# Kernel optimization log

Hardware: AMD Instinct MI355X
Metric: run time of the kernel (lower is better)

## Reference

```python
import jax, jax.numpy as jnp
import numpy as np

SEQ_LEN, BATCH, NUM_GROUPS, GROUP = 12, 512, 16, 32
H, E, MLP, BOTTLE, PRE = 128, 64, 1024, 1024, 512


def _pool_net(h, pos, num_groups, Wp, bp, W1, b1, W2, b2):
    # PoolHiddenNet: for each scene group, pairwise relative positions -> MLP -> max over neighbors
    B = h.shape[0]
    G = B // num_groups
    hg = h.reshape(num_groups, G, -1)          # (NG, G, H)
    pg = pos.reshape(num_groups, G, 2)         # (NG, G, 2)
    rel = pg[:, None, :, :] - pg[:, :, None, :]  # [g,i,j] = pos_j - pos_i
    emb = rel @ Wp.T + bp                      # (NG, G, G, E)
    hj = jnp.broadcast_to(hg[:, None, :, :], (num_groups, G, G, hg.shape[-1]))
    feats = jnp.concatenate([emb, hj], axis=-1)  # (NG, G, G, E+H)
    x = jax.nn.relu(feats @ W1.T + b1)         # (NG, G, G, 512)
    x = jax.nn.relu(x @ W2.T + b2)             # (NG, G, G, 1024)
    return x.max(axis=2).reshape(B, -1)        # max over neighbors j


def setup_inputs() -> dict:
    key = jax.random.key(0)
    ks = jax.random.split(key, 24)
    s = 0.05
    starts = np.arange(NUM_GROUPS, dtype=np.int64) * GROUP
    seq_start_end = jnp.asarray(np.stack([starts, starts + GROUP], axis=1))
    return {
        "last_pos": jax.random.normal(ks[0], (BATCH, 2), jnp.float32),
        "last_pos_rel": jax.random.normal(ks[1], (BATCH, 2), jnp.float32),
        "hh": jax.random.normal(ks[2], (1, BATCH, H), jnp.float32),
        "ch": jax.random.normal(ks[3], (1, BATCH, H), jnp.float32),
        "pred_traj_rel": jax.random.normal(ks[4], (SEQ_LEN, BATCH, 2), jnp.float32),
        "seq_start_end": seq_start_end,
        # LSTM (torch layout: gates ordered i,f,g,o)
        "W_ih": jax.random.normal(ks[5], (4 * H, E), jnp.float32) * s,
        "W_hh": jax.random.normal(ks[6], (4 * H, H), jnp.float32) * s,
        "b_ih": jax.random.normal(ks[7], (4 * H,), jnp.float32) * s,
        "b_hh": jax.random.normal(ks[8], (4 * H,), jnp.float32) * s,
        # spatial_embedding Linear(2, E)
        "Wse": jax.random.normal(ks[9], (E, 2), jnp.float32) * s,
        "bse": jax.random.normal(ks[10], (E,), jnp.float32) * s,
        # hidden2pos Linear(H, 2)
        "Wpos": jax.random.normal(ks[11], (2, H), jnp.float32) * s,
        "bpos": jax.random.normal(ks[12], (2,), jnp.float32) * s,
        # pool_net spatial_embedding Linear(2, E)
        "Wp": jax.random.normal(ks[13], (E, 2), jnp.float32) * s,
        "bp": jax.random.normal(ks[14], (E,), jnp.float32) * s,
        # pool_net mlp_pre_pool: [E+H, 512, BOTTLE], relu after each linear
        "W1": jax.random.normal(ks[15], (PRE, E + H), jnp.float32) * s,
        "b1": jax.random.normal(ks[16], (PRE,), jnp.float32) * s,
        "W2": jax.random.normal(ks[17], (BOTTLE, PRE), jnp.float32) * s,
        "b2": jax.random.normal(ks[18], (BOTTLE,), jnp.float32) * s,
        # decoder mlp: [H+BOTTLE, MLP, H], relu after each linear
        "Wm1": jax.random.normal(ks[19], (MLP, H + BOTTLE), jnp.float32) * s,
        "bm1": jax.random.normal(ks[20], (MLP,), jnp.float32) * s,
        "Wm2": jax.random.normal(ks[21], (H, MLP), jnp.float32) * s,
        "bm2": jax.random.normal(ks[22], (H,), jnp.float32) * s,
    }


def reference(last_pos, last_pos_rel, hh, ch, pred_traj_rel, seq_start_end,
              W_ih, W_hh, b_ih, b_hh, Wse, bse, Wpos, bpos,
              Wp, bp, W1, b1, W2, b2, Wm1, bm1, Wm2, bm2):
    num_groups = seq_start_end.shape[0]
    h0, c0 = hh[0], ch[0]
    dec_in0 = last_pos_rel @ Wse.T + bse

    def step(carry, gt_rel):
        last_pos_c, h, c, dec_in, loss = carry
        # single-layer LSTM cell (torch gate order i,f,g,o)
        gates = dec_in @ W_ih.T + b_ih + h @ W_hh.T + b_hh
        i, f, g, o = jnp.split(gates, 4, axis=-1)
        c = jax.nn.sigmoid(f) * c + jax.nn.sigmoid(i) * jnp.tanh(g)
        h = jax.nn.sigmoid(o) * jnp.tanh(c)
        rel_pos = h @ Wpos.T + bpos
        curr_pos = rel_pos + last_pos_c
        # pool every timestep + mlp back down to h_dim, replaces hidden state
        pool_h = _pool_net(h, curr_pos, num_groups, Wp, bp, W1, b1, W2, b2)
        dh = jnp.concatenate([h, pool_h], axis=1)
        dh = jax.nn.relu(dh @ Wm1.T + bm1)
        h = jax.nn.relu(dh @ Wm2.T + bm2)
        # training mode: teacher forcing + MSE loss
        loss = loss + jnp.mean((rel_pos - gt_rel) ** 2)
        dec_in = gt_rel @ Wse.T + bse
        return (curr_pos, h, c, dec_in, loss), rel_pos

    init = (last_pos, h0, c0, dec_in0, jnp.float32(0.0))
    (_, _, _, _, loss), pred_traj = jax.lax.scan(step, init, pred_traj_rel)
    return pred_traj, loss
```

## Files before the change

### kernel.cpp

```cpp
#include <hip/hip_runtime.h>
#include <math.h>

#define BATCH 512
#define NG 16
#define GSZ 32
#define H 128
#define E 64
#define PRE 512
#define BOT 1024
#define MLPD 1024
#define SEQ 12
#define AK 1152

typedef __attribute__((ext_vector_type(8))) short bf16x8;
typedef __attribute__((ext_vector_type(4))) float f32x4;

union bf8pack { ushort s[8]; uint4 v; };

__device__ __forceinline__ unsigned short f2bf(float f) {
    unsigned u = __float_as_uint(f);
    u += 0x7FFF + ((u >> 16) & 1);
    return (unsigned short)(u >> 16);
}

__device__ __forceinline__ uint4 pack8(const float* s) {
    float4 a = *(const float4*)s, b = *(const float4*)(s + 4);
    bf8pack o;
    o.s[0] = f2bf(a.x); o.s[1] = f2bf(a.y); o.s[2] = f2bf(a.z); o.s[3] = f2bf(a.w);
    o.s[4] = f2bf(b.x); o.s[5] = f2bf(b.y); o.s[6] = f2bf(b.z); o.s[7] = f2bf(b.w);
    return o.v;
}

#define GLB(p) ((const __attribute__((address_space(1))) unsigned int*)(p))
#define LDS(p) ((__attribute__((address_space(3))) unsigned int*)(p))

#define U0 ((BOT * PRE) / 8)
#define U1 ((MLPD * AK) / 8)
#define U2 ((H * MLPD) / 8)
#define U3 ((PRE * H) / 8)
#define U4 (PRE)
#define U5 ((BATCH * H) / 4)
#define U5b ((BATCH * H) / 8)
#define U6 (BATCH * 2)
#define U7 ((512 * 128) / 8)
#define U8 (512)
#define PREP_TOT (U0 + U1 + U2 + U3 + U4 + U5 + U5b + U6 + U7 + U8 + 1)

__global__ void prep_kernel(
    const float* __restrict__ W2, const float* __restrict__ Wm1,
    const float* __restrict__ Wm2, const float* __restrict__ W1,
    const float* __restrict__ Wp, const float* __restrict__ bp, const float* __restrict__ b1,
    const float* __restrict__ ch, const float* __restrict__ hh, const float* __restrict__ last_pos,
    const float* __restrict__ Wih, const float* __restrict__ Whh,
    const float* __restrict__ bih, const float* __restrict__ bhh,
    const float* __restrict__ Wse, const float* __restrict__ bse,
    unsigned short* __restrict__ W2pk, unsigned short* __restrict__ Wm1pk,
    unsigned short* __restrict__ Wm2pk, unsigned short* __restrict__ W1pk,
    float* __restrict__ Wcx, float* __restrict__ Wcy, float* __restrict__ biash,
    float* __restrict__ cbuf, unsigned short* __restrict__ Ahpk, float* __restrict__ pos,
    unsigned short* __restrict__ Whpk,
    float* __restrict__ Wx0, float* __restrict__ Wx1, float* __restrict__ bx,
    float* __restrict__ loss)
{
    long idx = (long)blockIdx.x * 256 + threadIdx.x;
    if (idx < U0) {
        int u = (int)idx;
        int lane = u & 63, rest = u >> 6;
        int ksg = rest & 15, cg = rest >> 4;
        int col = cg * 16 + (lane & 15);
        int kk = ksg * 32 + (lane >> 4) * 8;
        *(uint4*)&W2pk[(size_t)u * 8] = pack8(&W2[(size_t)col * PRE + kk]);
        return;
    }
    idx -= U0;
    if (idx < U1) {
        int u = (int)idx;
        int lane = u & 63, rest = u >> 6;
        int ksg = rest % 36, cg = rest / 36;
        int col = cg * 16 + (lane & 15);
        int k = ksg * 32 + (lane >> 4) * 8;
        *(uint4*)&Wm1pk[(size_t)u * 8] = pack8(&Wm1[(size_t)col * AK + k]);
        return;
    }
    idx -= U1;
    if (idx < U2) {
        int u = (int)idx;
        int lane = u & 63, rest = u >> 6;
        int ksg = rest & 31, cg = rest >> 5;
        int col = cg * 16 + (lane & 15);
        int k = ksg * 32 + (lane >> 4) * 8;
        *(uint4*)&Wm2pk[(size_t)u * 8] = pack8(&Wm2[(size_t)col * MLPD + k]);
        return;
    }
    idx -= U2;
    if (idx < U3) {
        int u = (int)idx;
        int l16 = u & 15, quad = (u >> 4) & 3, nt = (u >> 6) & 3, ks = (u >> 8) & 3, w = u >> 10;
        int col = w * 64 + nt * 16 + l16;
        int k = ks * 32 + quad * 8;
        *(uint4*)&W1pk[(size_t)u * 8] = pack8(&W1[col * 192 + E + k]);
        return;
    }
    idx -= U3;
    if (idx < U4) {
        int p = (int)idx;
        float sx = 0.f, sy = 0.f, sb = 0.f;
#pragma unroll 8
        for (int e = 0; e < E; ++e) {
            float w = W1[p * 192 + e];
            sx += w * Wp[e * 2 + 0];
            sy += w * Wp[e * 2 + 1];
            sb += w * bp[e];
        }
        Wcx[p] = sx; Wcy[p] = sy; biash[p] = b1[p] + sb;
        return;
    }
    idx -= U4;
    if (idx < U5) { ((float4*)cbuf)[idx] = ((const float4*)ch)[idx]; return; }
    idx -= U5;
    if (idx < U5b) {
        int u = (int)idx;
        int lane = u & 63, rest = u >> 6;
        int ks = rest & 3, rowtile = rest >> 2;
        int row = rowtile * 16 + (lane & 15);
        int k = ks * 32 + (lane >> 4) * 8;
        *(uint4*)&Ahpk[(size_t)u * 8] = pack8(&hh[(size_t)row * H + k]);
        return;
    }
    idx -= U5b;
    if (idx < U6) { pos[idx] = last_pos[idx]; return; }
    idx -= U6;
    if (idx < U7) {
        int u = (int)idx;
        int l16 = u & 15, quad = (u >> 4) & 3, ks = (u >> 6) & 3, w = (u >> 8) & 7, g = u >> 11;
        int col = g * 128 + w * 16 + l16;
        int k = ks * 32 + quad * 8;
        *(uint4*)&Whpk[(size_t)u * 8] = pack8(&Whh[(size_t)col * H + k]);
        return;
    }
    idx -= U7;
    if (idx < U8) {
        int u = (int)idx;
        float sx = 0.f, sy = 0.f, sb = 0.f;
#pragma unroll 8
        for (int e = 0; e < E; ++e) {
            float w = Wih[u * E + e];
            sx += w * Wse[e * 2 + 0];
            sy += w * Wse[e * 2 + 1];
            sb += w * bse[e];
        }
        Wx0[u] = sx; Wx1[u] = sy; bx[u] = sb + bih[u] + bhh[u];
        return;
    }
    idx -= U8;
    if (idx == 0) *loss = 0.0f;
}

#define LROWS 16
__global__ __launch_bounds__(512) void lstm_hpart(
    int t,
    const float* __restrict__ relin, const float* __restrict__ gt,
    const unsigned short* __restrict__ Whpk,
    const float* __restrict__ Wx0, const float* __restrict__ Wx1, const float* __restrict__ bx,
    const float* __restrict__ Wpos, const float* __restrict__ bpos,
    const unsigned short* __restrict__ W1pk, const float* __restrict__ biash,
    const unsigned short* __restrict__ Ahpk, float* __restrict__ cbuf,
    unsigned short* __restrict__ Abf, float* __restrict__ Hpartf,
    float* __restrict__ pos, float* __restrict__ traj, float* __restrict__ loss)
{
    constexpr int LDHB = 136;
    constexpr int LDHF = 129;
    __shared__ __align__(16) unsigned short hnb[LROWS * LDHB];
    __shared__ float hnf[LROWS * LDHF];
    __shared__ float lred[8];
    const int blk = blockIdx.x;
    const int r0 = blk * LROWS;
    const int tid = threadIdx.x;
    const int lane = tid & 63, w = tid >> 6;
    const int quad = lane >> 4, l16 = lane & 15;

    f32x4 acc[4];
#pragma unroll
    for (int g4 = 0; g4 < 4; ++g4) acc[g4] = (f32x4)0.f;
#pragma unroll
    for (int ks = 0; ks < 4; ++ks) {
        bf16x8 af = *(const bf16x8*)&Ahpk[((size_t)(blk * 4 + ks) * 64 + lane) * 8];
#pragma unroll
        for (int gate = 0; gate < 4; ++gate) {
            bf16x8 bf = *(const bf16x8*)&Whpk[((size_t)((gate * 8 + w) * 4 + ks) * 64 + lane) * 8];
            acc[gate] = __builtin_amdgcn_mfma_f32_16x16x32_bf16(af, bf, acc[gate], 0, 0, 0);
        }
    }

    {
        int u = w * 16 + l16;
        float wx0[4], wx1[4], bxv[4];
#pragma unroll
        for (int gate = 0; gate < 4; ++gate) {
            int col = gate * 128 + u;
            wx0[gate] = Wx0[col]; wx1[gate] = Wx1[col]; bxv[gate] = bx[col];
        }
#pragma unroll
        for (int r = 0; r < 4; ++r) {
            int row = quad * 4 + r;
            int b = r0 + row;
            float rx = relin[b * 2 + 0], ry = relin[b * 2 + 1];
            float i_ = acc[0][r] + rx * wx0[0] + ry * wx1[0] + bxv[0];
            float f_ = acc[1][r] + rx * wx0[1] + ry * wx1[1] + bxv[1];
            float g_ = acc[2][r] + rx * wx0[2] + ry * wx1[2] + bxv[2];
            float o_ = acc[3][r] + rx * wx0[3] + ry * wx1[3] + bxv[3];
            float ig = 1.0f / (1.0f + expf(-i_));
            float fg = 1.0f / (1.0f + expf(-f_));
            float gg = tanhf(g_);
            float og = 1.0f / (1.0f + expf(-o_));
            float c = fg * cbuf[(size_t)b * H + u] + ig * gg;
            cbuf[(size_t)b * H + u] = c;
            float h = og * tanhf(c);
            hnb[row * LDHB + u] = f2bf(h);
            hnf[row * LDHF + u] = h;
            Abf[(size_t)b * AK + u] = f2bf(h);
        }
    }
    __syncthreads();

    if (t < SEQ - 1) {
        f32x4 acc2[4];
#pragma unroll
        for (int nt = 0; nt < 4; ++nt) acc2[nt] = (f32x4)0.f;
#pragma unroll
        for (int ks = 0; ks < 4; ++ks) {
            bf16x8 af = *(const bf16x8*)&hnb[l16 * LDHB + ks * 32 + quad * 8];
#pragma unroll
            for (int nt = 0; nt < 4; ++nt) {
                bf16x8 bfr = *(const bf16x8*)&W1pk[((size_t)((w * 4 + ks) * 4 + nt) * 64 + lane) * 8];
                acc2[nt] = __builtin_amdgcn_mfma_f32_16x16x32_bf16(af, bfr, acc2[nt], 0, 0, 0);
            }
        }
#pragma unroll
        for (int nt = 0; nt < 4; ++nt) {
            int col = w * 64 + nt * 16 + l16;
            float bv = biash[col];
#pragma unroll
            for (int r = 0; r < 4; ++r) {
                int row = quad * 4 + r;
                Hpartf[(size_t)(r0 + row) * PRE + col] = acc2[nt][r] + bv;
            }
        }
    }

    {
        int row = tid >> 5, o = (tid >> 4) & 1, seg = tid & 15;
        const float* wr = Wpos + o * H + seg * 8;
        const float* hr = &hnf[row * LDHF + seg * 8];
        float acc3 = 0.f;
#pragma unroll
        for (int k = 0; k < 8; ++k) acc3 += wr[k] * hr[k];
        acc3 += __shfl_xor(acc3, 1);
        acc3 += __shfl_xor(acc3, 2);
        acc3 += __shfl_xor(acc3, 4);
        acc3 += __shfl_xor(acc3, 8);
        acc3 += bpos[o];
        int b = r0 + row;
        float d = acc3 - gt[b * 2 + o];
        if (seg == 0) {
            float lp = pos[b * 2 + o];
            pos[b * 2 + o] = acc3 + lp;
            traj[b * 2 + o] = acc3;
        }
        float part = (seg == 0) ? d * d : 0.f;
        part += __shfl_xor(part, 16);
        part += __shfl_xor(part, 32);
        if (lane == 0) lred[w] = part;
        __syncthreads();
        if (tid == 0) {
            float s = 0.f;
#pragma unroll
            for (int i = 0; i < 8; ++i) s += lred[i];
            atomicAdd(loss, s * (1.0f / 1024.0f));
        }
    }
}

template <int BM, int BN, int KW, int NW, int MODE>
__global__ __launch_bounds__(256) void gemm_splitk_pk(
    const unsigned short* __restrict__ A, int lda,
    const unsigned short* __restrict__ Bpk, int K,
    const float* __restrict__ bias,
    float* __restrict__ Cf, unsigned short* __restrict__ Cb, int ldc)
{
    constexpr int MT = BM / 16;
    constexpr int NT = BN / (16 * NW);
    constexpr int ABUF = KW * BM * 64;
    __shared__ __align__(16) unsigned short As[2 * ABUF];
    __shared__ float red[KW * BM * BN];
    int tid = threadIdx.x;
    int lane = tid & 63, w = tid >> 6;
    int kslice = w / NW, nslice = w % NW;
    int gtid = tid & (NW * 64 - 1);
    int quad = lane >> 4, l16 = lane & 15;
    int m0 = blockIdx.y * BM, n0 = blockIdx.x * BN;
    const int KC = K / KW;
    const int NK = KC / 64;
    const int KSGT = K >> 5;
    const int cgbase = (n0 + nslice * (BN / NW)) >> 4;

    auto STAGE = [&](int ki, int bo) {
        int kb = kslice * KC + ki * 64;
#pragma unroll
        for (int u = 0; u < BM / (8 * NW); ++u) {
            int c = u * NW * 64 + gtid;
            __builtin_amdgcn_global_load_lds(
                GLB(A + (size_t)(m0 + (c >> 3)) * lda + kb + (c & 7) * 8),
                LDS(&As[bo + kslice * BM * 64 + c * 8]), 16, 0, 0);
        }
    };

    f32x4 acc[MT][NT];
#pragma unroll
    for (int mt = 0; mt < MT; ++mt)
#pragma unroll
        for (int nt = 0; nt < NT; ++nt) acc[mt][nt] = (f32x4)0.f;

    STAGE(0, 0);
    for (int ki = 0; ki < NK; ++ki) {
        int bo = (ki & 1) * ABUF;
        int kgbase = (kslice * KC + ki * 64) >> 5;
        __syncthreads();
#pragma unroll
        for (int ks = 0; ks < 2; ++ks) {
            bf16x8 af[MT], bfr[NT];
#pragma unroll
            for (int mt = 0; mt < MT; ++mt)
                af[mt] = *(const bf16x8*)&As[bo + kslice * BM * 64 + (mt * 16 + l16) * 64 + ks * 32 + quad * 8];
#pragma unroll
            for (int nt = 0; nt < NT; ++nt)
                bfr[nt] = *(const bf16x8*)&Bpk[((size_t)((cgbase + nt) * KSGT + kgbase + ks) * 64 + lane) * 8];
#pragma unroll
            for (int mt = 0; mt < MT; ++mt)
#pragma unroll
                for (int nt = 0; nt < NT; ++nt)
                    acc[mt][nt] = __builtin_amdgcn_mfma_f32_16x16x32_bf16(af[mt], bfr[nt], acc[mt][nt], 0, 0, 0);
        }
        if (ki + 1 < NK) STAGE(ki + 1, ((ki + 1) & 1) * ABUF);
    }

#pragma unroll
    for (int mt = 0; mt < MT; ++mt)
#pragma unroll
    for (int nt = 0; nt < NT; ++nt) {
#pragma unroll
        for (int r = 0; r < 4; ++r) {
            int row = mt * 16 + quad * 4 + r;
            int col = nslice * (BN / NW) + nt * 16 + l16;
            red[kslice * BM * BN + row * BN + col] = acc[mt][nt][r];
        }
    }
    __syncthreads();

#pragma unroll
    for (int o = 0; o < BM * BN / 256; ++o) {
        int e = o * 256 + tid;
        int row = e / BN, col = e % BN;
        float s = 0.f;
#pragma unroll
        for (int k = 0; k < KW; ++k) s += red[k * BM * BN + e];
        float v = fmaxf(s + bias[n0 + col], 0.f);
        if (MODE == 1) {
            Cb[(size_t)(m0 + row) * ldc + n0 + col] = f2bf(v);
        } else if (MODE == 2) {
            Cf[(size_t)(m0 + row) * ldc + n0 + col] = v;
        } else {
            int gr = m0 + row, gc = n0 + col;
            int rowtile = gr >> 4, l16p = gr & 15;
            int ksv = gc >> 5, quadp = (gc >> 3) & 3, ep = gc & 7;
            int lanep = quadp * 16 + l16p;
            Cb[((size_t)(rowtile * 4 + ksv) * 64 + lanep) * 8 + ep] = f2bf(v);
        }
    }
}

__global__ __launch_bounds__(512) void pool_fused(
    const float* __restrict__ Hpartf, const float* __restrict__ pos,
    const float* __restrict__ Wcx, const float* __restrict__ Wcy,
    const unsigned short* __restrict__ W2pk,
    const float* __restrict__ b2, unsigned short* __restrict__ Abf)
{
    constexpr int LDA = 72;
    constexpr int ASZ = 128 * LDA;
    __shared__ __align__(16) unsigned short As[2 * ASZ];
    const int tid = threadIdx.x;
    const int lane = tid & 63, w = tid >> 6;
    const int quad = lane >> 4, l16 = lane & 15;
    const int n_tile = blockIdx.x, m_tile = blockIdx.y;
    const int g = m_tile >> 3, iq = m_tile & 7;
    const int n0 = n_tile * 512;

    const int brow = tid >> 2;
    const int k8 = (tid & 3) * 16;
    const int bi = iq * 4 + (brow >> 5), bj = brow & 31;
    const float rx = pos[(g * GSZ + bj) * 2 + 0] - pos[(g * GSZ + bi) * 2 + 0];
    const float ry = pos[(g * GSZ + bj) * 2 + 1] - pos[(g * GSZ + bi) * 2 + 1];
    const float* hrow = &Hpartf[(size_t)(g * GSZ + bj) * PRE];

    auto BUILD = [&](int k0i, unsigned short* dst) {
        const int k0 = k0i * 64;
        const float4* hp = (const float4*)(hrow + k0 + k8);
        const float4* wx = (const float4*)(Wcx + k0 + k8);
        const float4* wy = (const float4*)(Wcy + k0 + k8);
        bf8pack o[2];
#pragma unroll
        for (int q = 0; q < 2; ++q) {
            float4 ha = hp[q * 2], hb = hp[q * 2 + 1];
            float4 xa = wx[q * 2], xb = wx[q * 2 + 1];
            float4 ya = wy[q * 2], yb = wy[q * 2 + 1];
            o[q].s[0] = f2bf(fmaxf(ha.x + rx * xa.x + ry * ya.x, 0.f));
            o[q].s[1] = f2bf(fmaxf(ha.y + rx * xa.y + ry * ya.y, 0.f));
            o[q].s[2] = f2bf(fmaxf(ha.z + rx * xa.z + ry * ya.z, 0.f));
            o[q].s[3] = f2bf(fmaxf(ha.w + rx * xa.w + ry * ya.w, 0.f));
            o[q].s[4] = f2bf(fmaxf(hb.x + rx * xb.x + ry * yb.x, 0.f));
            o[q].s[5] = f2bf(fmaxf(hb.y + rx * xb.y + ry * yb.y, 0.f));
            o[q].s[6] = f2bf(fmaxf(hb.z + rx * xb.z + ry * yb.z, 0.f));
            o[q].s[7] = f2bf(fmaxf(hb.w + rx * xb.w + ry * yb.w, 0.f));
        }
        *(uint4*)&dst[brow * LDA + k8] = o[0].v;
        *(uint4*)&dst[brow * LDA + k8 + 8] = o[1].v;
    };

    f32x4 acc[8][4];
#pragma unroll
    for (int mt = 0; mt < 8; ++mt)
#pragma unroll
        for (int nt = 0; nt < 4; ++nt) acc[mt][nt] = (f32x4)0.f;

    BUILD(0, As);
    for (int k0i = 0; k0i < 8; ++k0i) {
        unsigned short* cur = As + (k0i & 1) * ASZ;
        __syncthreads();
        __builtin_amdgcn_s_setprio(1);
#pragma unroll
        for (int ks = 0; ks < 2; ++ks) {
            bf16x8 bfr[4];
#pragma unroll
            for (int nt = 0; nt < 4; ++nt) {
                int cg = n_tile * 32 + w * 4 + nt;
                int ksg = k0i * 2 + ks;
                bfr[nt] = *(const bf16x8*)&W2pk[((size_t)(cg * 16 + ksg) * 64 + lane) * 8];
            }
#pragma unroll
            for (int mt = 0; mt < 8; ++mt) {
                bf16x8 af = *(const bf16x8*)&cur[(mt * 16 + l16) * LDA + ks * 32 + quad * 8];
#pragma unroll
                for (int nt = 0; nt < 4; ++nt)
                    acc[mt][nt] = __builtin_amdgcn_mfma_f32_16x16x32_bf16(af, bfr[nt], acc[mt][nt], 0, 0, 0);
            }
        }
        __builtin_amdgcn_s_setprio(0);
        if (k0i < 7) BUILD(k0i + 1, As + ((k0i + 1) & 1) * ASZ);
    }

#pragma unroll
    for (int il = 0; il < 4; ++il)
#pragma unroll
    for (int nt = 0; nt < 4; ++nt) {
        float u = -1e30f;
#pragma unroll
        for (int p = 0; p < 2; ++p)
#pragma unroll
            for (int r = 0; r < 4; ++r) u = fmaxf(u, acc[il * 2 + p][nt][r]);
        u = fmaxf(u, __shfl_xor(u, 16));
        u = fmaxf(u, __shfl_xor(u, 32));
        if (lane < 16) {
            int col = n0 + w * 64 + nt * 16 + l16;
            int gu = m_tile * 4 + il;
            Abf[(size_t)gu * AK + H + col] = f2bf(fmaxf(u + b2[col], 0.f));
        }
    }
}

extern "C" void kernel_launch(void* const* d_in, const int* in_sizes, int n_in,
                              void* d_out, int out_size, void* d_ws, size_t ws_size,
                              hipStream_t stream)
{
    const float* last_pos     = (const float*)d_in[0];
    const float* last_pos_rel = (const float*)d_in[1];
    const float* hh           = (const float*)d_in[2];
    const float* ch           = (const float*)d_in[3];
    const float* ptr_rel      = (const float*)d_in[4];
    const float* Wih  = (const float*)d_in[6];
    const float* Whh  = (const float*)d_in[7];
    const float* bih  = (const float*)d_in[8];
    const float* bhh  = (const float*)d_in[9];
    const float* Wse  = (const float*)d_in[10];
    const float* bse  = (const float*)d_in[11];
    const float* Wpos = (const float*)d_in[12];
    const float* bpos = (const float*)d_in[13];
    const float* Wp   = (const float*)d_in[14];
    const float* bp   = (const float*)d_in[15];
    const float* W1   = (const float*)d_in[16];
    const float* b1   = (const float*)d_in[17];
    const float* W2   = (const float*)d_in[18];
    const float* b2   = (const float*)d_in[19];
    const float* Wm1  = (const float*)d_in[20];
    const float* bm1  = (const float*)d_in[21];
    const float* Wm2  = (const float*)d_in[22];
    const float* bm2  = (const float*)d_in[23];

    float* ws     = (float*)d_ws;
    unsigned short* Ahpk = (unsigned short*)ws;
    float* cbuf   = ws + BATCH * H;
    float* pos    = cbuf + BATCH * H;
    float* Hpartf = pos + 1024;
    float* Wcx    = Hpartf + BATCH * PRE;
    float* Wcy    = Wcx + PRE;
    float* biash  = Wcy + PRE;
    float* bx     = biash + PRE;
    float* Wx0    = bx + 512;
    float* Wx1    = Wx0 + 512;
    unsigned short* ub    = (unsigned short*)(Wx1 + 512);
    unsigned short* Abf   = ub;
    unsigned short* dhbf  = Abf + (size_t)BATCH * AK;
    unsigned short* W2pk  = dhbf + (size_t)BATCH * MLPD;
    unsigned short* Wm1pk = W2pk + (size_t)BOT * PRE;
    unsigned short* Wm2pk = Wm1pk + (size_t)MLPD * AK;
    unsigned short* W1pk  = Wm2pk + (size_t)H * MLPD;
    unsigned short* Whpk  = W1pk + (size_t)PRE * H;

    float* out  = (float*)d_out;
    float* loss = out + SEQ * BATCH * 2;

    prep_kernel<<<(PREP_TOT + 255) / 256, 256, 0, stream>>>(
        W2, Wm1, Wm2, W1, Wp, bp, b1, ch, hh, last_pos, Wih, Whh, bih, bhh, Wse, bse,
        W2pk, Wm1pk, Wm2pk, W1pk, Wcx, Wcy, biash, cbuf, Ahpk, pos, Whpk, Wx0, Wx1, bx, loss);

    for (int t = 0; t < SEQ; t++) {
        const float* relin = (t == 0) ? last_pos_rel : (ptr_rel + (t - 1) * BATCH * 2);
        const float* gt = ptr_rel + t * BATCH * 2;
        lstm_hpart<<<BATCH / LROWS, 512, 0, stream>>>(t, relin, gt, Whpk, Wx0, Wx1, bx,
                                                      Wpos, bpos, W1pk, biash, Ahpk, cbuf,
                                                      Abf, Hpartf, pos,
                                                      out + t * BATCH * 2, loss);
        if (t == SEQ - 1) break;
        pool_fused<<<dim3(2, 128), 512, 0, stream>>>(Hpartf, pos, Wcx, Wcy, W2pk, b2, Abf);
        gemm_splitk_pk<64, 32, 2, 2, 1><<<dim3(MLPD / 32, BATCH / 64), 256, 0, stream>>>(
            Abf, AK, Wm1pk, AK, bm1, nullptr, dhbf, MLPD);
        gemm_splitk_pk<16, 32, 4, 1, 3><<<dim3(H / 32, BATCH / 16), 256, 0, stream>>>(
            dhbf, MLPD, Wm2pk, MLPD, bm2, nullptr, Ahpk, H);
    }
}
```

Before: 665.1 us.

## Fuse second MLP GEMM into next-step LSTM kernel to drop a launch

Folds the Wm2 GEMM (dh -> h) into the following timestep's LSTM kernel. Each 16-row block now computes its new hidden state with MFMA over the full K=1024 and stages it in shared memory, so the packed hidden-state round trip through global memory and one kernel launch per step go away. The Wm1 GEMM now writes its output in MFMA-packed layout, which needed the packed-store index to use ldc. The cost is more serial K-loop work per block with no split-K, and each block reloads the Wm2 weights.

```diff
diff --git a/kernel.cpp b/kernel.cpp
--- a/kernel.cpp
+++ b/kernel.cpp
@@ -156,35 +156,26 @@
     if (idx == 0) *loss = 0.0f;
 }
 
-#define LROWS 16
-__global__ __launch_bounds__(512) void lstm_hpart(
-    int t,
-    const float* __restrict__ relin, const float* __restrict__ gt,
-    const unsigned short* __restrict__ Whpk,
-    const float* __restrict__ Wx0, const float* __restrict__ Wx1, const float* __restrict__ bx,
-    const float* __restrict__ Wpos, const float* __restrict__ bpos,
-    const unsigned short* __restrict__ W1pk, const float* __restrict__ biash,
-    const unsigned short* __restrict__ Ahpk, float* __restrict__ cbuf,
-    unsigned short* __restrict__ Abf, float* __restrict__ Hpartf,
-    float* __restrict__ pos, float* __restrict__ traj, float* __restrict__ loss)
+__device__ __forceinline__ void lstm_body(
+    int s, int r0, int tid, int lane, int w, int quad, int l16,
+    unsigned short* hmb , unsigned short* hnb, float* hnf, float* lred,
+    const float* relin, const float* gt,
+    const unsigned short* Whpk,
+    const float* Wx0, const float* Wx1, const float* bx,
+    const float* Wpos, const float* bpos,
+    const unsigned short* W1pk, const float* biash,
+    float* cbuf, unsigned short* Abf, float* Hpartf,
+    float* pos, float* traj, float* loss)
 {
     constexpr int LDHB = 136;
     constexpr int LDHF = 129;
-    __shared__ __align__(16) unsigned short hnb[LROWS * LDHB];
-    __shared__ float hnf[LROWS * LDHF];
-    __shared__ float lred[8];
-    const int blk = blockIdx.x;
-    const int r0 = blk * LROWS;
-    const int tid = threadIdx.x;
-    const int lane = tid & 63, w = tid >> 6;
-    const int quad = lane >> 4, l16 = lane & 15;
 
     f32x4 acc[4];
 #pragma unroll
     for (int g4 = 0; g4 < 4; ++g4) acc[g4] = (f32x4)0.f;
 #pragma unroll
     for (int ks = 0; ks < 4; ++ks) {
-        bf16x8 af = *(const bf16x8*)&Ahpk[((size_t)(blk * 4 + ks) * 64 + lane) * 8];
+        bf16x8 af = *(const bf16x8*)&hmb[l16 * LDHB + ks * 32 + quad * 8];
 #pragma unroll
         for (int gate = 0; gate < 4; ++gate) {
             bf16x8 bf = *(const bf16x8*)&Whpk[((size_t)((gate * 8 + w) * 4 + ks) * 64 + lane) * 8];
@@ -223,7 +214,7 @@
     }
     __syncthreads();
 
-    if (t < SEQ - 1) {
+    if (s < SEQ - 1) {
         f32x4 acc2[4];
 #pragma unroll
         for (int nt = 0; nt < 4; ++nt) acc2[nt] = (f32x4)0.f;
@@ -273,12 +264,89 @@
         if (lane == 0) lred[w] = part;
         __syncthreads();
         if (tid == 0) {
-            float s = 0.f;
-#pragma unroll
-            for (int i = 0; i < 8; ++i) s += lred[i];
-            atomicAdd(loss, s * (1.0f / 1024.0f));
-        }
-    }
+            float s2 = 0.f;
+#pragma unroll
+            for (int i = 0; i < 8; ++i) s2 += lred[i];
+            atomicAdd(loss, s2 * (1.0f / 1024.0f));
+        }
+    }
+}
+
+#define LROWS 16
+__global__ __launch_bounds__(512) void lstm_hpart(
+    const float* __restrict__ relin, const float* __restrict__ gt,
+    const unsigned short* __restrict__ Whpk,
+    const float* __restrict__ Wx0, const float* __restrict__ Wx1, const float* __restrict__ bx,
+    const float* __restrict__ Wpos, const float* __restrict__ bpos,
+    const unsigned short* __restrict__ W1pk, const float* __restrict__ biash,
+    const unsigned short* __restrict__ Ahpk, float* __restrict__ cbuf,
+    unsigned short* __restrict__ Abf, float* __restrict__ Hpartf,
+    float* __restrict__ pos, float* __restrict__ traj, float* __restrict__ loss)
+{
+    constexpr int LDHB = 136;
+    constexpr int LDHF = 129;
+    __shared__ __align__(16) unsigned short hmb[LROWS * LDHB];
+    __shared__ __align__(16) unsigned short hnb[LROWS * LDHB];
+    __shared__ float hnf[LROWS * LDHF];
+    __shared__ float lred[8];
+    const int blk = blockIdx.x, tid = threadIdx.x;
+    const int lane = tid & 63, w = tid >> 6;
+    const int quad = lane >> 4, l16 = lane & 15;
+
+    for (int e2 = tid; e2 < LROWS * H / 8; e2 += 512) {
+        int lane2 = e2 & 63, ks = e2 >> 6;
+        int row = lane2 & 15, k = ks * 32 + (lane2 >> 4) * 8;
+        *(uint4*)&hmb[row * LDHB + k] = *(const uint4*)&Ahpk[((size_t)(blk * 4 + ks) * 64 + lane2) * 8];
+    }
+    __syncthreads();
+
+    lstm_body(0, blk * LROWS, tid, lane, w, quad, l16, hmb, hnb, hnf, lred,
+              relin, gt, Whpk, Wx0, Wx1, bx, Wpos, bpos, W1pk, biash,
+              cbuf, Abf, Hpartf, pos, traj, loss);
+}
+
+__global__ __launch_bounds__(512) void mlp2_lstm(
+    int s,
+    const unsigned short* __restrict__ dhpk,
+    const unsigned short* __restrict__ Wm2pk, const float* __restrict__ bm2,
+    const float* __restrict__ relin, const float* __restrict__ gt,
+    const unsigned short* __restrict__ Whpk,
+    const float* __restrict__ Wx0, const float* __restrict__ Wx1, const float* __restrict__ bx,
+    const float* __restrict__ Wpos, const float* __restrict__ bpos,
+    const unsigned short* __restrict__ W1pk, const float* __restrict__ biash,
+    float* __restrict__ cbuf,
+    unsigned short* __restrict__ Abf, float* __restrict__ Hpartf,
+    float* __restrict__ pos, float* __restrict__ traj, float* __restrict__ loss)
+{
+    constexpr int LDHB = 136;
+    constexpr int LDHF = 129;
+    __shared__ __align__(16) unsigned short hmb[LROWS * LDHB];
+    __shared__ __align__(16) unsigned short hnb[LROWS * LDHB];
+    __shared__ float hnf[LROWS * LDHF];
+    __shared__ float lred[8];
+    const int blk = blockIdx.x, tid = threadIdx.x;
+    const int lane = tid & 63, w = tid >> 6;
+    const int quad = lane >> 4, l16 = lane & 15;
+
+    f32x4 acc0 = (f32x4)0.f;
+#pragma unroll 8
+    for (int ki = 0; ki < 32; ++ki) {
+        bf16x8 af = *(const bf16x8*)&dhpk[((size_t)(blk * 32 + ki) * 64 + lane) * 8];
+        bf16x8 bf = *(const bf16x8*)&Wm2pk[((size_t)(w * 32 + ki) * 64 + lane) * 8];
+        acc0 = __builtin_amdgcn_mfma_f32_16x16x32_bf16(af, bf, acc0, 0, 0, 0);
+    }
+    {
+        int u = w * 16 + l16;
+        float bv = bm2[u];
+#pragma unroll
+        for (int r = 0; r < 4; ++r)
+            hmb[(quad * 4 + r) * LDHB + u] = f2bf(fmaxf(acc0[r] + bv, 0.f));
+    }
+    __syncthreads();
+
+    lstm_body(s, blk * LROWS, tid, lane, w, quad, l16, hmb, hnb, hnf, lred,
+              relin, gt, Whpk, Wx0, Wx1, bx, Wpos, bpos, W1pk, biash,
+              cbuf, Abf, Hpartf, pos, traj, loss);
 }
 
 template <int BM, int BN, int KW, int NW, int MODE>
@@ -374,7 +442,7 @@
             int rowtile = gr >> 4, l16p = gr & 15;
             int ksv = gc >> 5, quadp = (gc >> 3) & 3, ep = gc & 7;
             int lanep = quadp * 16 + l16p;
-            Cb[((size_t)(rowtile * 4 + ksv) * 64 + lanep) * 8 + ep] = f2bf(v);
+            Cb[((size_t)(rowtile * (ldc >> 5) + ksv) * 64 + lanep) * 8 + ep] = f2bf(v);
         }
     }
 }
@@ -518,8 +586,8 @@
     float* Wx1    = Wx0 + 512;
     unsigned short* ub    = (unsigned short*)(Wx1 + 512);
     unsigned short* Abf   = ub;
-    unsigned short* dhbf  = Abf + (size_t)BATCH * AK;
-    unsigned short* W2pk  = dhbf + (size_t)BATCH * MLPD;
+    unsigned short* dhpk  = Abf + (size_t)BATCH * AK;
+    unsigned short* W2pk  = dhpk + (size_t)BATCH * MLPD;
     unsigned short* Wm1pk = W2pk + (size_t)BOT * PRE;
     unsigned short* Wm2pk = Wm1pk + (size_t)MLPD * AK;
     unsigned short* W1pk  = Wm2pk + (size_t)H * MLPD;
@@ -532,18 +600,18 @@
         W2, Wm1, Wm2, W1, Wp, bp, b1, ch, hh, last_pos, Wih, Whh, bih, bhh, Wse, bse,
         W2pk, Wm1pk, Wm2pk, W1pk, Wcx, Wcy, biash, cbuf, Ahpk, pos, Whpk, Wx0, Wx1, bx, loss);
 
-    for (int t = 0; t < SEQ; t++) {
-        const float* relin = (t == 0) ? last_pos_rel : (ptr_rel + (t - 1) * BATCH * 2);
-        const float* gt = ptr_rel + t * BATCH * 2;
-        lstm_hpart<<<BATCH / LROWS, 512, 0, stream>>>(t, relin, gt, Whpk, Wx0, Wx1, bx,
-                                                      Wpos, bpos, W1pk, biash, Ahpk, cbuf,
-                                                      Abf, Hpartf, pos,
-                                                      out + t * BATCH * 2, loss);
-        if (t == SEQ - 1) break;
+    lstm_hpart<<<BATCH / LROWS, 512, 0, stream>>>(
+        last_pos_rel, ptr_rel, Whpk, Wx0, Wx1, bx, Wpos, bpos, W1pk, biash,
+        Ahpk, cbuf, Abf, Hpartf, pos, out, loss);
+
+    for (int t = 0; t < SEQ - 1; t++) {
         pool_fused<<<dim3(2, 128), 512, 0, stream>>>(Hpartf, pos, Wcx, Wcy, W2pk, b2, Abf);
-        gemm_splitk_pk<64, 32, 2, 2, 1><<<dim3(MLPD / 32, BATCH / 64), 256, 0, stream>>>(
-            Abf, AK, Wm1pk, AK, bm1, nullptr, dhbf, MLPD);
-        gemm_splitk_pk<16, 32, 4, 1, 3><<<dim3(H / 32, BATCH / 16), 256, 0, stream>>>(
-            dhbf, MLPD, Wm2pk, MLPD, bm2, nullptr, Ahpk, H);
-    }
-}
+        gemm_splitk_pk<64, 32, 2, 2, 3><<<dim3(MLPD / 32, BATCH / 64), 256, 0, stream>>>(
+            Abf, AK, Wm1pk, AK, bm1, nullptr, dhpk, MLPD);
+        mlp2_lstm<<<BATCH / LROWS, 512, 0, stream>>>(
+            t + 1, dhpk, Wm2pk, bm2,
+            ptr_rel + t * BATCH * 2, ptr_rel + (t + 1) * BATCH * 2,
+            Whpk, Wx0, Wx1, bx, Wpos, bpos, W1pk, biash,
+            cbuf, Abf, Hpartf, pos, out + (t + 1) * BATCH * 2, loss);
+    }
+}
```

Result: faster. 645.0 us (-3.0%).
